# Kernel tuning notes

Hardware: AMD Instinct MI355X
Metric: run time of the kernel (lower is better)

## Reference

```python
import jax, jax.numpy as jnp
import numpy as np

ALPHA = 0.1  # cfg.model.mmd.attention_temperature
EPS = 1e-12


def _l2norm(x, axis=-1):
    return x / jnp.sqrt(jnp.sum(x * x, axis=axis, keepdims=True) + EPS)


def setup_inputs() -> dict:
    key = jax.random.key(0)
    k1, k2, k3, k4 = jax.random.split(key, 4)
    b, ng, nl, nf, c = 8, 5, 75, 196, 640
    return {
        "global_f": jax.random.normal(k1, (b, ng, c), dtype=jnp.float32),
        "local_f": jax.random.normal(k2, (b, nl, nf, c), dtype=jnp.float32),
        "Wq": jax.random.normal(k3, (c, c), dtype=jnp.float32) / np.sqrt(c),
        "Wk": jax.random.normal(k4, (c, c), dtype=jnp.float32) / np.sqrt(c),
    }


def reference(global_f, local_f, Wq, Wk):
    # AttentiveMMDPrompt.compute_attn_weight with dim=1, num_groups=1.
    b, ng, c = global_f.shape
    _, nl, nf, _ = local_f.shape
    # q/k projections (nn.Linear, no bias): x @ W^T
    g = jnp.einsum('bgc,dc->bgd', global_f, Wq)          # [b, ng, c]
    l = jnp.einsum('blfc,dc->blfd', local_f, Wk)         # [b, nl, nf, c]
    # centering: subtract joint per-episode mean feature over all tokens
    tot = g.sum(axis=1) + l.sum(axis=(1, 2))             # [b, c]
    mean = tot / (ng + nl * nf)
    g = g - mean[:, None, :]
    l = l - mean[:, None, None, :]
    # l2 normalize feature vectors
    g = _l2norm(g)
    l = _l2norm(l)
    # score: local_f @ global_f -> [b, nl, ng, nf]
    scores = jnp.einsum('blfc,bgc->blgf', l, g) / ALPHA
    attn = jax.nn.softmax(scores, axis=-1)               # softmax over nf
    return attn[..., None]                               # [b, nl, ng, nf, 1]
```

## Files before the change

kernel.cpp:

```cpp
#include <hip/hip_runtime.h>
#include <math.h>

namespace {
constexpr int kB = 8, kNG = 5, kNL = 75, kNF = 196, kC = 640;
constexpr int kNTokL = kNL * kNF;
constexpr int kNTot = kNG + kNTokL;
constexpr float kEps = 1e-12f;
constexpr float kInvAlpha = 10.0f;
constexpr int kKC = 20;
constexpr int kTiles = 230;
constexpr int kNT = 5;
}

typedef __attribute__((ext_vector_type(8))) short short8;
typedef __attribute__((ext_vector_type(4))) short short4v;
typedef __attribute__((ext_vector_type(4))) float floatx4;

union S8U { short8 v; ushort u[8]; };
union S4U { short4v v; ushort u[4]; };

__device__ __forceinline__ void bsplit(float x, ushort& h, ushort& l) {
  union { float f; uint u; } a; a.f = x;
  uint uh = (a.u + 0x7FFFu + ((a.u >> 16) & 1u)) >> 16;
  h = (ushort)uh;
  union { uint u; float f; } bb; bb.u = uh << 16;
  float r = x - bb.f;
  union { float f; uint u; } c; c.f = r;
  l = (ushort)((c.u + 0x7FFFu + ((c.u >> 16) & 1u)) >> 16);
}

#define MFMA_BF16(a, b, c) __builtin_amdgcn_mfma_f32_16x16x32_bf16(a, b, c, 0, 0, 0)

__device__ __forceinline__ void bar_lds() {
  asm volatile("s_waitcnt lgkmcnt(0)\n\ts_barrier" ::: "memory");
}


__global__ void k_sum_local(const float* __restrict__ lf, float* __restrict__ s_l) {
  const int b = blockIdx.x, slice = blockIdx.y;
  const int tid = threadIdx.x;
  const int c4 = tid % 160, h = tid / 160;
  const int t0 = slice * 230 + h * 115;
  const int nrow = min(115, kNTokL - t0);
  const float* p = lf + ((size_t)b * kNTokL + t0) * kC + c4 * 4;
  float4 acc = {0.f, 0.f, 0.f, 0.f};
  for (int i = 0; i < nrow; ++i) {
    const float4 v = *(const float4*)(p + (size_t)i * kC);
    acc.x += v.x; acc.y += v.y; acc.z += v.z; acc.w += v.w;
  }
  float* dst = &s_l[b * kC + c4 * 4];
  atomicAdd(dst + 0, acc.x);
  atomicAdd(dst + 1, acc.y);
  atomicAdd(dst + 2, acc.z);
  atomicAdd(dst + 3, acc.w);
}

__global__ void k_cvtW(const float* __restrict__ Wk, ushort* __restrict__ Wh,
                       ushort* __restrict__ Wl) {
  const int wv = blockIdx.x * 4 + (threadIdx.x >> 6);
  const int lane = threadIdx.x & 63;
  const int kc = wv % kKC, dt = wv / kKC;
  const int fm = lane & 15, quad = lane >> 4;
  const float* p = Wk + (size_t)(dt * 16 + fm) * kC + kc * 32 + quad * 8;
  float4 a = *(const float4*)p;
  float4 c = *(const float4*)(p + 4);
  S8U h, l;
  bsplit(a.x, h.u[0], l.u[0]); bsplit(a.y, h.u[1], l.u[1]);
  bsplit(a.z, h.u[2], l.u[2]); bsplit(a.w, h.u[3], l.u[3]);
  bsplit(c.x, h.u[4], l.u[4]); bsplit(c.y, h.u[5], l.u[5]);
  bsplit(c.z, h.u[6], l.u[6]); bsplit(c.w, h.u[7], l.u[7]);
  const size_t off = ((size_t)dt * kKC + kc) * 512 + (size_t)lane * 8;
  *(short8*)(Wh + off) = h.v;
  *(short8*)(Wl + off) = l.v;
}

__global__ void k_proj_mean(const float* __restrict__ Wq, const float* __restrict__ Wk,
                            const float* __restrict__ gf, const float* __restrict__ s_l,
                            float* __restrict__ m, float* __restrict__ gc) {
  const int wid = blockIdx.x * 4 + (threadIdx.x >> 6);
  const int lane = threadIdx.x & 63;
  const int b = wid / kC, d = wid % kC;
  float ak = 0.f, ag[kNG] = {0.f, 0.f, 0.f, 0.f, 0.f};
  for (int c = lane; c < kC; c += 64) {
    const float wq = Wq[d * kC + c];
    const float wk = Wk[d * kC + c];
    ak += wk * s_l[b * kC + c];
#pragma unroll
    for (int g = 0; g < kNG; ++g) ag[g] += wq * gf[(b * kNG + g) * kC + c];
  }
#pragma unroll
  for (int off = 32; off > 0; off >>= 1) {
    ak += __shfl_xor(ak, off);
#pragma unroll
    for (int g = 0; g < kNG; ++g) ag[g] += __shfl_xor(ag[g], off);
  }
  if (lane == 0) {
    float aq = 0.f;
#pragma unroll
    for (int g = 0; g < kNG; ++g) aq += ag[g];
    const float mv = (aq + ak) / (float)kNTot;
    m[b * kC + d] = mv;
#pragma unroll
    for (int g = 0; g < kNG; ++g) gc[(b * kNG + g) * kC + d] = ag[g] - mv;
  }
}

__global__ void k_norm_g(const float* __restrict__ gc, float* __restrict__ gn) {
  const int row = blockIdx.x;
  __shared__ float red[256];
  float a = 0.f;
  for (int d = threadIdx.x; d < kC; d += 256) {
    const float v = gc[row * kC + d];
    a += v * v;
  }
  red[threadIdx.x] = a;
  __syncthreads();
  for (int s = 128; s > 0; s >>= 1) {
    if (threadIdx.x < s) red[threadIdx.x] += red[threadIdx.x + s];
    __syncthreads();
  }
  const float rs = 1.0f / sqrtf(red[0] + kEps);
  for (int d = threadIdx.x; d < kC; d += 256) gn[row * kC + d] = gc[row * kC + d] * rs;
}

__global__ __launch_bounds__(512, 1) void k_big(
    const float* __restrict__ lf, const ushort* __restrict__ Wh,
    const ushort* __restrict__ Wl, const float* __restrict__ m,
    const float* __restrict__ gn, float* __restrict__ scores) {
  __shared__ char smem[16384];
  ushort* Ah0 = (ushort*)smem;
  ushort* Al0 = (ushort*)(smem + 4096);
  ushort* Ah1 = (ushort*)(smem + 8192);
  ushort* Al1 = (ushort*)(smem + 12288);
  float* red = (float*)smem;

  const int tid = threadIdx.x;
  const int wn = tid >> 6, lane = tid & 63;
  const int fm = lane & 15, quad = lane >> 4;
  const int b = blockIdx.x & 7, tile = blockIdx.x >> 3;
  const int tok0 = tile * 64;

  const int sr = tid >> 3, sq = tid & 7;
  const int st = tok0 + sr;
  const bool sok = st < kNTokL;
  const float* xrow = lf + ((size_t)b * kNTokL + st) * kC + sq * 4;
  const int aoff = ((sr >> 4) << 9) + (((sq >> 1) * 16 + (sr & 15)) << 3) + ((sq & 1) << 2);

  const ushort* bhbase = Wh + ((size_t)wn * kNT * kKC) * 512 + (size_t)lane * 8;
  const ushort* blbase = Wl + ((size_t)wn * kNT * kKC) * 512 + (size_t)lane * 8;

  floatx4 acc[4][kNT];
#pragma unroll
  for (int i = 0; i < 4; ++i)
#pragma unroll
    for (int j = 0; j < kNT; ++j) acc[i][j] = (floatx4){0.f, 0.f, 0.f, 0.f};

#define STAGE_A(XV, AH, AL)                                   \
  {                                                           \
    S4U _h, _l;                                               \
    bsplit((XV).x, _h.u[0], _l.u[0]);                         \
    bsplit((XV).y, _h.u[1], _l.u[1]);                         \
    bsplit((XV).z, _h.u[2], _l.u[2]);                         \
    bsplit((XV).w, _h.u[3], _l.u[3]);                         \
    *(short4v*)((AH) + aoff) = _h.v;                          \
    *(short4v*)((AL) + aoff) = _l.v;                          \
  }

#define LOADB(BH, BL, KCI)                                                        \
  {                                                                               \
    _Pragma("unroll") for (int nt = 0; nt < kNT; ++nt) {                          \
      BH[nt] = *(const short8*)(bhbase + ((size_t)nt * kKC + (KCI)) * 512);       \
      BL[nt] = *(const short8*)(blbase + ((size_t)nt * kKC + (KCI)) * 512);       \
    }                                                                             \
  }

#define READA(AH, AL)                                                  \
  {                                                                    \
    _Pragma("unroll") for (int mt = 0; mt < 4; ++mt) {                 \
      ah[mt] = *(const short8*)((AH) + mt * 512 + lane * 8);           \
      al[mt] = *(const short8*)((AL) + mt * 512 + lane * 8);           \
    }                                                                  \
  }

#define DOMFMA(BH, BL)                                                 \
  {                                                                    \
    _Pragma("unroll") for (int nt = 0; nt < kNT; ++nt)                 \
        _Pragma("unroll") for (int mt = 0; mt < 4; ++mt) {             \
      acc[mt][nt] = MFMA_BF16(ah[mt], BH[nt], acc[mt][nt]);            \
      acc[mt][nt] = MFMA_BF16(al[mt], BH[nt], acc[mt][nt]);            \
      acc[mt][nt] = MFMA_BF16(ah[mt], BL[nt], acc[mt][nt]);            \
    }                                                                  \
  }

  const float4 fzero = {0.f, 0.f, 0.f, 0.f};
  float4 x0 = sok ? *(const float4*)xrow : fzero;
  STAGE_A(x0, Ah0, Al0);
  float4 xA = sok ? *(const float4*)(xrow + 32) : fzero;
  float4 xB = fzero;
  short8 BH0[kNT], BL0[kNT], BH1[kNT], BL1[kNT];
  LOADB(BH0, BL0, 0);

  short8 ah[4], al[4];
  for (int kc = 0; kc < kKC; kc += 2) {
    bar_lds();
    READA(Ah0, Al0);
    LOADB(BH1, BL1, kc + 1);
    if (sok && kc + 2 < kKC) xB = *(const float4*)(xrow + (kc + 2) * 32);
    STAGE_A(xA, Ah1, Al1);
    DOMFMA(BH0, BL0);

    bar_lds();
    READA(Ah1, Al1);
    if (kc + 2 < kKC) {
      LOADB(BH0, BL0, kc + 2);
      if (sok && kc + 3 < kKC) xA = *(const float4*)(xrow + (kc + 3) * 32);
      STAGE_A(xB, Ah0, Al0);
    }
    DOMFMA(BH1, BL1);
  }

  float mv[kNT], gvv[5][kNT];
#pragma unroll
  for (int nt = 0; nt < kNT; ++nt) {
    const int d = wn * 80 + nt * 16 + fm;
    mv[nt] = m[b * kC + d];
#pragma unroll
    for (int g = 0; g < 5; ++g) gvv[g][nt] = gn[(b * kNG + g) * kC + d];
  }

  bar_lds();
#pragma unroll
  for (int mt = 0; mt < 4; ++mt)
#pragma unroll
    for (int reg = 0; reg < 4; ++reg) {
      float part[6] = {0.f, 0.f, 0.f, 0.f, 0.f, 0.f};
#pragma unroll
      for (int nt = 0; nt < kNT; ++nt) {
        const float yc = acc[mt][nt][reg] - mv[nt];
        part[0] += yc * yc;
#pragma unroll
        for (int g = 0; g < 5; ++g) part[1 + g] += yc * gvv[g][nt];
      }
#pragma unroll
      for (int off = 1; off < 16; off <<= 1)
#pragma unroll
        for (int v = 0; v < 6; ++v) part[v] += __shfl_xor(part[v], off);
      if (fm == 0) {
        const int row = mt * 16 + quad * 4 + reg;
#pragma unroll
        for (int v = 0; v < 6; ++v) red[((size_t)wn * 64 + row) * 6 + v] = part[v];
      }
    }
  bar_lds();
  if (tid < 64) {
    const int tok = tok0 + tid;
    if (tok < kNTokL) {
      float s[6] = {0.f, 0.f, 0.f, 0.f, 0.f, 0.f};
#pragma unroll
      for (int w = 0; w < 8; ++w)
#pragma unroll
        for (int v = 0; v < 6; ++v) s[v] += red[((size_t)w * 64 + tid) * 6 + v];
      const float rs = (1.0f / sqrtf(s[0] + kEps)) * kInvAlpha;
      const size_t t = (size_t)b * kNTokL + tok;
#pragma unroll
      for (int g = 0; g < 5; ++g)
        scores[(size_t)g * (kB * kNTokL) + t] = s[1 + g] * rs;
    }
  }
#undef STAGE_A
#undef LOADB
#undef READA
#undef DOMFMA
}

__global__ void k_softmax(const float* __restrict__ scores, float* __restrict__ out) {
  const int wid = blockIdx.x * 4 + (threadIdx.x >> 6);
  const int lane = threadIdx.x & 63;
  const int b = wid / (kNL * kNG);
  const int rem = wid % (kNL * kNG);
  const int l = rem / kNG, g = rem % kNG;
  float sv[4];
  float mx = -1e30f;
#pragma unroll
  for (int u = 0; u < 4; ++u) {
    const int f = lane + 64 * u;
    if (f < kNF) {
      const size_t t = (size_t)b * kNTokL + (size_t)l * kNF + f;
      sv[u] = scores[(size_t)g * (kB * kNTokL) + t];
      mx = fmaxf(mx, sv[u]);
    } else {
      sv[u] = 0.f;
    }
  }
#pragma unroll
  for (int off = 32; off > 0; off >>= 1) mx = fmaxf(mx, __shfl_xor(mx, off));
  float se = 0.f;
#pragma unroll
  for (int u = 0; u < 4; ++u) {
    const int f = lane + 64 * u;
    const float e = (f < kNF) ? expf(sv[u] - mx) : 0.f;
    sv[u] = e;
    se += e;
  }
#pragma unroll
  for (int off = 32; off > 0; off >>= 1) se += __shfl_xor(se, off);
  const float inv = 1.0f / se;
#pragma unroll
  for (int u = 0; u < 4; ++u) {
    const int f = lane + 64 * u;
    if (f < kNF) out[((size_t)(b * kNL + l) * kNG + g) * kNF + f] = sv[u] * inv;
  }
}


extern "C" void kernel_launch(void* const* d_in, const int* in_sizes, int n_in,
                              void* d_out, int out_size, void* d_ws, size_t ws_size,
                              hipStream_t stream) {
  (void)in_sizes; (void)n_in; (void)out_size; (void)ws_size;
  const float* gf = (const float*)d_in[0];
  const float* lf = (const float*)d_in[1];
  const float* Wq = (const float*)d_in[2];
  const float* Wk = (const float*)d_in[3];
  float* ws = (float*)d_ws;
  float* out = (float*)d_out;

  float* s_l    = ws;
  float* m      = ws + 5120;
  float* gc     = ws + 10240;
  float* gn     = ws + 35840;
  float* scores = ws + 61440;
  ushort* Wh    = (ushort*)(ws + 649440);
  ushort* Wl    = (ushort*)(ws + 854240);

  hipMemsetAsync(s_l, 0, (size_t)5120 * 4, stream);

  k_sum_local<<<dim3(kB, 64), 320, 0, stream>>>(lf, s_l);
  k_cvtW<<<200, 256, 0, stream>>>(Wk, Wh, Wl);
  k_proj_mean<<<(kB * kC) / 4, 256, 0, stream>>>(Wq, Wk, gf, s_l, m, gc);
  k_norm_g<<<kB * kNG, 256, 0, stream>>>(gc, gn);
  k_big<<<kTiles * kB, 512, 0, stream>>>(lf, Wh, Wl, m, gn, scores);
  k_softmax<<<750, 256, 0, stream>>>(scores, out);
}
```

Before: 766.1 us.

## Widen A-staging to 8 elements per thread, regroup MFMAs, double sum-local grid

In the main GEMM kernel, only the first 256 threads now stage the A tile. Each of them loads two float4s, splits eight values into bf16 hi/lo and writes short8 to LDS instead of short4. The three split-bf16 MFMA passes are reordered so each pass runs over all tiles before the next, which removes back-to-back dependent accumulations on the same register. The local-sum reduction kernel uses twice as many blocks with shorter row ranges per thread to raise parallelism, at the cost of more atomics.

```diff
diff --git a/kernel.cpp b/kernel.cpp
--- a/kernel.cpp
+++ b/kernel.cpp
@@ -13,11 +13,9 @@
 }
 
 typedef __attribute__((ext_vector_type(8))) short short8;
-typedef __attribute__((ext_vector_type(4))) short short4v;
 typedef __attribute__((ext_vector_type(4))) float floatx4;
 
 union S8U { short8 v; ushort u[8]; };
-union S4U { short4v v; ushort u[4]; };
 
 __device__ __forceinline__ void bsplit(float x, ushort& h, ushort& l) {
   union { float f; uint u; } a; a.f = x;
@@ -40,12 +38,13 @@
   const int b = blockIdx.x, slice = blockIdx.y;
   const int tid = threadIdx.x;
   const int c4 = tid % 160, h = tid / 160;
-  const int t0 = slice * 230 + h * 115;
-  const int nrow = min(115, kNTokL - t0);
+  const int t0 = slice * 115 + (h ? 58 : 0);
+  const int t1 = min(slice * 115 + (h ? 115 : 58), kNTokL);
   const float* p = lf + ((size_t)b * kNTokL + t0) * kC + c4 * 4;
   float4 acc = {0.f, 0.f, 0.f, 0.f};
-  for (int i = 0; i < nrow; ++i) {
-    const float4 v = *(const float4*)(p + (size_t)i * kC);
+  for (int t = t0; t < t1; ++t) {
+    const float4 v = *(const float4*)p;
+    p += kC;
     acc.x += v.x; acc.y += v.y; acc.z += v.z; acc.w += v.w;
   }
   float* dst = &s_l[b * kC + c4 * 4];
@@ -140,11 +139,10 @@
   const int b = blockIdx.x & 7, tile = blockIdx.x >> 3;
   const int tok0 = tile * 64;
 
-  const int sr = tid >> 3, sq = tid & 7;
-  const int st = tok0 + sr;
-  const bool sok = st < kNTokL;
-  const float* xrow = lf + ((size_t)b * kNTokL + st) * kC + sq * 4;
-  const int aoff = ((sr >> 4) << 9) + (((sq >> 1) * 16 + (sr & 15)) << 3) + ((sq & 1) << 2);
+  const int sr = tid >> 2, sq = tid & 3;
+  const bool stg = tid < 256 && (tok0 + sr) < kNTokL;
+  const float* xrow = lf + ((size_t)b * kNTokL + tok0 + sr) * kC + sq * 8;
+  const int aoff = ((sr >> 4) << 9) + ((sq * 16 + (sr & 15)) << 3);
 
   const ushort* bhbase = Wh + ((size_t)wn * kNT * kKC) * 512 + (size_t)lane * 8;
   const ushort* blbase = Wl + ((size_t)wn * kNT * kKC) * 512 + (size_t)lane * 8;
@@ -155,15 +153,19 @@
 #pragma unroll
     for (int j = 0; j < kNT; ++j) acc[i][j] = (floatx4){0.f, 0.f, 0.f, 0.f};
 
-#define STAGE_A(XV, AH, AL)                                   \
-  {                                                           \
-    S4U _h, _l;                                               \
-    bsplit((XV).x, _h.u[0], _l.u[0]);                         \
-    bsplit((XV).y, _h.u[1], _l.u[1]);                         \
-    bsplit((XV).z, _h.u[2], _l.u[2]);                         \
-    bsplit((XV).w, _h.u[3], _l.u[3]);                         \
-    *(short4v*)((AH) + aoff) = _h.v;                          \
-    *(short4v*)((AL) + aoff) = _l.v;                          \
+#define STAGE_A(X0, X1, AH, AL)                               \
+  if (stg) {                                                  \
+    S8U _h, _l;                                               \
+    bsplit((X0).x, _h.u[0], _l.u[0]);                         \
+    bsplit((X0).y, _h.u[1], _l.u[1]);                         \
+    bsplit((X0).z, _h.u[2], _l.u[2]);                         \
+    bsplit((X0).w, _h.u[3], _l.u[3]);                         \
+    bsplit((X1).x, _h.u[4], _l.u[4]);                         \
+    bsplit((X1).y, _h.u[5], _l.u[5]);                         \
+    bsplit((X1).z, _h.u[6], _l.u[6]);                         \
+    bsplit((X1).w, _h.u[7], _l.u[7]);                         \
+    *(short8*)((AH) + aoff) = _h.v;                           \
+    *(short8*)((AL) + aoff) = _l.v;                           \
   }
 
 #define LOADB(BH, BL, KCI)                                                        \
@@ -185,18 +187,23 @@
 #define DOMFMA(BH, BL)                                                 \
   {                                                                    \
     _Pragma("unroll") for (int nt = 0; nt < kNT; ++nt)                 \
-        _Pragma("unroll") for (int mt = 0; mt < 4; ++mt) {             \
-      acc[mt][nt] = MFMA_BF16(ah[mt], BH[nt], acc[mt][nt]);            \
-      acc[mt][nt] = MFMA_BF16(al[mt], BH[nt], acc[mt][nt]);            \
-      acc[mt][nt] = MFMA_BF16(ah[mt], BL[nt], acc[mt][nt]);            \
-    }                                                                  \
+        _Pragma("unroll") for (int mt = 0; mt < 4; ++mt)               \
+            acc[mt][nt] = MFMA_BF16(ah[mt], BH[nt], acc[mt][nt]);      \
+    _Pragma("unroll") for (int nt = 0; nt < kNT; ++nt)                 \
+        _Pragma("unroll") for (int mt = 0; mt < 4; ++mt)               \
+            acc[mt][nt] = MFMA_BF16(al[mt], BH[nt], acc[mt][nt]);      \
+    _Pragma("unroll") for (int nt = 0; nt < kNT; ++nt)                 \
+        _Pragma("unroll") for (int mt = 0; mt < 4; ++mt)               \
+            acc[mt][nt] = MFMA_BF16(ah[mt], BL[nt], acc[mt][nt]);      \
   }
 
   const float4 fzero = {0.f, 0.f, 0.f, 0.f};
-  float4 x0 = sok ? *(const float4*)xrow : fzero;
-  STAGE_A(x0, Ah0, Al0);
-  float4 xA = sok ? *(const float4*)(xrow + 32) : fzero;
-  float4 xB = fzero;
+  float4 x0a = fzero, x0b = fzero, xA0 = fzero, xA1 = fzero, xB0 = fzero, xB1 = fzero;
+  if (stg) {
+    x0a = *(const float4*)xrow;       x0b = *(const float4*)(xrow + 4);
+    xA0 = *(const float4*)(xrow + 32); xA1 = *(const float4*)(xrow + 36);
+  }
+  STAGE_A(x0a, x0b, Ah0, Al0);
   short8 BH0[kNT], BL0[kNT], BH1[kNT], BL1[kNT];
   LOADB(BH0, BL0, 0);
 
@@ -205,16 +212,22 @@
     bar_lds();
     READA(Ah0, Al0);
     LOADB(BH1, BL1, kc + 1);
-    if (sok && kc + 2 < kKC) xB = *(const float4*)(xrow + (kc + 2) * 32);
-    STAGE_A(xA, Ah1, Al1);
+    if (stg && kc + 2 < kKC) {
+      xB0 = *(const float4*)(xrow + (kc + 2) * 32);
+      xB1 = *(const float4*)(xrow + (kc + 2) * 32 + 4);
+    }
+    STAGE_A(xA0, xA1, Ah1, Al1);
     DOMFMA(BH0, BL0);
 
     bar_lds();
     READA(Ah1, Al1);
     if (kc + 2 < kKC) {
       LOADB(BH0, BL0, kc + 2);
-      if (sok && kc + 3 < kKC) xA = *(const float4*)(xrow + (kc + 3) * 32);
-      STAGE_A(xB, Ah0, Al0);
+      if (stg && kc + 3 < kKC) {
+        xA0 = *(const float4*)(xrow + (kc + 3) * 32);
+        xA1 = *(const float4*)(xrow + (kc + 3) * 32 + 4);
+      }
+      STAGE_A(xB0, xB1, Ah0, Al0);
     }
     DOMFMA(BH1, BL1);
   }
@@ -334,7 +347,7 @@
 
   hipMemsetAsync(s_l, 0, (size_t)5120 * 4, stream);
 
-  k_sum_local<<<dim3(kB, 64), 320, 0, stream>>>(lf, s_l);
+  k_sum_local<<<dim3(kB, 128), 320, 0, stream>>>(lf, s_l);
   k_cvtW<<<200, 256, 0, stream>>>(Wk, Wh, Wl);
   k_proj_mean<<<(kB * kC) / 4, 256, 0, stream>>>(Wq, Wk, gf, s_l, m, gc);
   k_norm_g<<<kB * kNG, 256, 0, stream>>>(gc, gn);
```

Result: slower. 896.0 us (+17.0%).
